# Optimization experiments

Measured on AMD Instinct MI355X. Metric: run time of the kernel, lower is better.

## Reference

```python
import jax, jax.numpy as jnp
import numpy as np

HID = 128      # hidden_dim
CDIM = 128     # c_dim
NBLK = 5       # n_blocks
RESO = 32      # grid_resolution
G = RESO ** 3  # number of voxels
B, T = 2, 100000


def setup_inputs() -> dict:
    key = jax.random.key(0)
    ks = jax.random.split(key, 8)
    return {
        "points": jax.random.normal(ks[0], (B, T, 3), jnp.float32),
        "index": jax.random.randint(ks[1], (B, 1, T), 0, G, dtype=jnp.int64),
        # fc_pos: Linear(3, 2*HID)
        "fc_pos_w": jax.random.normal(ks[2], (3, 2 * HID), jnp.float32) * 0.1,
        "fc_pos_b": jnp.zeros((2 * HID,), jnp.float32),
        # ResnetBlockFC(2*HID, HID) x NBLK: fc_0 (2H->H), fc_1 (H->H), shortcut (2H->H, no bias)
        "fc0_w": jax.random.normal(ks[3], (NBLK, 2 * HID, HID), jnp.float32) * 0.05,
        "fc0_b": jnp.zeros((NBLK, HID), jnp.float32),
        "fc1_w": jax.random.normal(ks[4], (NBLK, HID, HID), jnp.float32) * 0.05,
        "fc1_b": jnp.zeros((NBLK, HID), jnp.float32),
        "sc_w": jax.random.normal(ks[5], (NBLK, 2 * HID, HID), jnp.float32) * 0.05,
        # fc_c: Linear(HID, CDIM)
        "fc_c_w": jax.random.normal(ks[6], (HID, CDIM), jnp.float32) * 0.05,
        "fc_c_b": jnp.zeros((CDIM,), jnp.float32),
    }


def _resnet_block(x, w0, b0, w1, b1, ws):
    # ResnetBlockFC: net = fc_0(relu(x)); dx = fc_1(relu(net)); out = shortcut(x) + dx
    net = jnp.maximum(x, 0.0) @ w0 + b0
    dx = jnp.maximum(net, 0.0) @ w1 + b1
    return x @ ws + dx


def reference(points, index, fc_pos_w, fc_pos_b, fc0_w, fc0_b, fc1_w, fc1_b, sc_w, fc_c_w, fc_c_b):
    idx = index[:, 0, :]  # [B, T]

    def pool_local(net):
        # scatter_max over voxels, then gather back per point
        seg = jax.vmap(lambda c_b, i_b: jax.ops.segment_max(c_b, i_b, num_segments=G))(net, idx)  # [B,G,H]
        return jnp.take_along_axis(seg, idx[:, :, None], axis=1)  # [B,T,H]; every gathered voxel is non-empty

    net = points @ fc_pos_w + fc_pos_b          # [B,T,2H]
    net = _resnet_block(net, fc0_w[0], fc0_b[0], fc1_w[0], fc1_b[0], sc_w[0])  # [B,T,H]
    for i in range(1, NBLK):
        pooled = pool_local(net)
        net = jnp.concatenate([net, pooled], axis=2)  # [B,T,2H]
        net = _resnet_block(net, fc0_w[i], fc0_b[i], fc1_w[i], fc1_b[i], sc_w[i])

    c = net @ fc_c_w + fc_c_b  # [B,T,CDIM]

    # generate_grid_features: scatter_mean into the 32^3 grid (zeros for empty voxels)
    sums = jax.vmap(lambda c_b, i_b: jax.ops.segment_sum(c_b, i_b, num_segments=G))(c, idx)  # [B,G,CDIM]
    cnts = jax.vmap(lambda i_b: jax.ops.segment_sum(jnp.ones((T,), c.dtype), i_b, num_segments=G))(idx)  # [B,G]
    cnts = cnts[:, :, None]
    mean = jnp.where(cnts > 0, sums / jnp.maximum(cnts, 1.0), 0.0)
    fea_grid = jnp.transpose(mean, (0, 2, 1)).reshape(B, CDIM, RESO, RESO, RESO)
    return fea_grid
```

## Files before the change

### kernel.cpp

```cpp
#include <hip/hip_runtime.h>

#define T_PTS 100000
#define NB 2
#define NROWS (NB * T_PTS)
#define GCELLS 32768
#define NCELL (NB * GCELLS)
#define HID 128
#define MBLK 64
#define GRID_RB (NROWS / MBLK)

typedef __attribute__((ext_vector_type(8))) short bf16x8;
typedef __attribute__((ext_vector_type(4))) float f32x4;

#define MFMA16 __builtin_amdgcn_mfma_f32_16x16x32_bf16

__device__ __forceinline__ unsigned short bf16rne(float f) {
  unsigned u = __float_as_uint(f);
  return (unsigned short)((u + 0x7FFFu + ((u >> 16) & 1u)) >> 16);
}
__device__ __forceinline__ void bf16split(float f, unsigned short& h,
                                          unsigned short& l) {
  h = bf16rne(f);
  l = bf16rne(f - __uint_as_float(((unsigned)h) << 16));
}
__device__ __forceinline__ unsigned packhl(float f) {
  unsigned short h, l;
  bf16split(f, h, l);
  return (((unsigned)h) << 16) | (unsigned)l;
}

union U8 { bf16x8 v; unsigned u[4]; };

__device__ __forceinline__ void up2(unsigned w0, unsigned w1, unsigned& h,
                                    unsigned& l) {
  h = __builtin_amdgcn_perm(w1, w0, 0x07060302u);
  l = __builtin_amdgcn_perm(w1, w0, 0x05040100u);
}

__device__ __forceinline__ void relu2(unsigned qh, unsigned ql, unsigned& rh,
                                      unsigned& rl) {
  const unsigned keep = ((~qh >> 15) & 0x00010001u) * 0xFFFFu;
  rh = qh & keep;
  rl = ql & keep;
}

__device__ __forceinline__ void dma16(const unsigned* g, unsigned* l) {
  __builtin_amdgcn_global_load_lds(
      (const __attribute__((address_space(1))) unsigned*)g,
      (__attribute__((address_space(3))) unsigned*)l, 16, 0, 0);
}

template <int MODE>
__global__ __launch_bounds__(256, 4) void resblock_mfma(
    const void* __restrict__ srcv, const float* __restrict__ posw,
    const float* __restrict__ posb, const unsigned* __restrict__ cell,
    const int* __restrict__ perm, const int* __restrict__ vcell,
    const unsigned short* __restrict__ w0p, const float* __restrict__ b0,
    const unsigned short* __restrict__ w1p, const float* __restrict__ b1,
    const unsigned short* __restrict__ swp, unsigned* __restrict__ net_out) {
  __shared__ unsigned lds32[8192];
  const int tid = threadIdx.x;
  const int lane = tid & 63;
  const int wid = tid >> 6;
  const int wc = wid;
  const int t0 = blockIdx.x * MBLK;

  const int srow = wid * 16 + (lane & 15);
  const int skc4 = (lane >> 4) * 4;
  const long vrow = (long)t0 + srow;
  const unsigned* nrowL = nullptr;
  const unsigned* crowL = nullptr;
  float pp0 = 0.f, pp1 = 0.f, pp2 = 0.f;
  if (MODE == 1) {
    nrowL = (const unsigned*)srcv + vrow * HID;
    crowL = cell + (long)vcell[vrow] * HID;
  } else {
    const float* ppp = (const float*)srcv + (long)perm[vrow] * 3;
    pp0 = ppp[0]; pp1 = ppp[1]; pp2 = ppp[2];
  }

  auto stage_dma = [&](int ks) {
    unsigned* base = &lds32[((ks & 1) << 11) + wid * 256];
    const unsigned* rowp = (ks < 4) ? nrowL : crowL;
    const int ko = ((ks & 3) << 4) + skc4;
    dma16(rowp + ko, base);
    dma16(rowp + 64 + ko, base + 1024);
  };
  auto stage0 = [&](int ks) {
    const int kb = ks * 32 + (lane >> 4) * 8;
    float xv[8];
#pragma unroll
    for (int i = 0; i < 8; i += 4) {
      float4 wa = *(const float4*)(posw + kb + i);
      float4 wb = *(const float4*)(posw + 256 + kb + i);
      float4 wcc = *(const float4*)(posw + 512 + kb + i);
      float4 bb = *(const float4*)(posb + kb + i);
      xv[i + 0] = fmaf(pp0, wa.x, fmaf(pp1, wb.x, fmaf(pp2, wcc.x, bb.x)));
      xv[i + 1] = fmaf(pp0, wa.y, fmaf(pp1, wb.y, fmaf(pp2, wcc.y, bb.y)));
      xv[i + 2] = fmaf(pp0, wa.z, fmaf(pp1, wb.z, fmaf(pp2, wcc.z, bb.z)));
      xv[i + 3] = fmaf(pp0, wa.w, fmaf(pp1, wb.w, fmaf(pp2, wcc.w, bb.w)));
    }
    unsigned ph[8];
#pragma unroll
    for (int i = 0; i < 8; ++i) ph[i] = packhl(xv[i]);
    uint4 xh4, xl4;
    up2(ph[0], ph[1], xh4.x, xl4.x);
    up2(ph[2], ph[3], xh4.y, xl4.y);
    up2(ph[4], ph[5], xh4.z, xl4.z);
    up2(ph[6], ph[7], xh4.w, xl4.w);
    const int db = ((ks & 1) << 11) + wid * 256 + lane * 4;
    *(uint4*)&lds32[db] = xh4;
    *(uint4*)&lds32[db + 1024] = xl4;
  };
  auto load_B = [&](const unsigned short* base, int loOff, int ks, bf16x8* h,
                    bf16x8* l) {
#pragma unroll
    for (int nt = 0; nt < 2; ++nt) {
      const int fi = (ks * 8 + wc * 2 + nt) * 512 + lane * 8;
      h[nt] = *(const bf16x8*)(base + fi);
      l[nt] = *(const bf16x8*)(base + loOff + fi);
    }
  };

  f32x4 accy[4][2], acco[4][2];
#pragma unroll
  for (int i = 0; i < 4; ++i)
#pragma unroll
    for (int j = 0; j < 2; ++j) {
      f32x4 z = {0.f, 0.f, 0.f, 0.f};
      accy[i][j] = z;
      acco[i][j] = z;
    }

  if (MODE == 1) {
    stage_dma(0);
  } else {
    stage0(0);
  }
  __syncthreads();

#pragma unroll 1
  for (int ks = 0; ks < 8; ++ks) {
    const int sb = (ks & 1) << 11;
    bf16x8 b1h[2], b1l[2], b2h[2], b2l[2];
    load_B(w0p, 32768, ks, b1h, b1l);
    load_B(swp, 32768, ks, b2h, b2l);
    if (MODE == 1 && ks < 7) stage_dma(ks + 1);
    __builtin_amdgcn_s_setprio(1);
#pragma unroll
    for (int mt = 0; mt < 4; ++mt) {
      const unsigned* px = &lds32[sb + mt * 256 + lane * 4];
      U8 xh, xl, rh, rl;
      xh.v = *(const bf16x8*)px;
      xl.v = *(const bf16x8*)(px + 1024);
#pragma unroll
      for (int i = 0; i < 4; ++i) relu2(xh.u[i], xl.u[i], rh.u[i], rl.u[i]);
#pragma unroll
      for (int nt = 0; nt < 2; ++nt) {
        accy[mt][nt] = MFMA16(rh.v, b1h[nt], accy[mt][nt], 0, 0, 0);
        accy[mt][nt] = MFMA16(rh.v, b1l[nt], accy[mt][nt], 0, 0, 0);
        accy[mt][nt] = MFMA16(rl.v, b1h[nt], accy[mt][nt], 0, 0, 0);
      }
#pragma unroll
      for (int nt = 0; nt < 2; ++nt) {
        acco[mt][nt] = MFMA16(xh.v, b2h[nt], acco[mt][nt], 0, 0, 0);
        acco[mt][nt] = MFMA16(xh.v, b2l[nt], acco[mt][nt], 0, 0, 0);
        acco[mt][nt] = MFMA16(xl.v, b2h[nt], acco[mt][nt], 0, 0, 0);
      }
    }
    __builtin_amdgcn_s_setprio(0);
    if (MODE == 0 && ks < 7) stage0(ks + 1);
    __syncthreads();
  }

  {
    float b0v[2];
#pragma unroll
    for (int nt = 0; nt < 2; ++nt)
      b0v[nt] = b0[wc * 32 + nt * 16 + (lane & 15)];
#pragma unroll
    for (int mt = 0; mt < 4; ++mt) {
#pragma unroll
      for (int nt = 0; nt < 2; ++nt) {
        const int c = wc * 32 + nt * 16 + (lane & 15);
        const int k2 = c >> 5;
        const int j = c & 7;
        const int lahi = ((c & 31) >> 3) * 16;
#pragma unroll
        for (int r = 0; r < 4; ++r) {
          float h = fmaxf(accy[mt][nt][r] + b0v[nt], 0.f);
          int la = lahi + (lane >> 4) * 4 + r;
          la ^= (la >> 3) & 7;
          lds32[((k2 * 4 + mt) * 64 + la) * 8 + j] = packhl(h);
        }
      }
    }
  }
  __syncthreads();

  {
    const int lar2 = lane ^ ((lane >> 3) & 7);
#pragma unroll
    for (int k2 = 0; k2 < 4; ++k2) {
      bf16x8 ch[2], cl[2];
      load_B(w1p, 16384, k2, ch, cl);
      __builtin_amdgcn_s_setprio(1);
#pragma unroll
      for (int mt = 0; mt < 4; ++mt) {
        const unsigned* p = &lds32[((k2 * 4 + mt) * 64 + lar2) * 8];
        uint4 q1 = *(const uint4*)p;
        uint4 q2 = *(const uint4*)(p + 4);
        unsigned q[8] = {q1.x, q1.y, q1.z, q1.w, q2.x, q2.y, q2.z, q2.w};
        U8 ah, al;
#pragma unroll
        for (int p2 = 0; p2 < 4; ++p2)
          up2(q[2 * p2], q[2 * p2 + 1], ah.u[p2], al.u[p2]);
#pragma unroll
        for (int nt = 0; nt < 2; ++nt) {
          acco[mt][nt] = MFMA16(ah.v, ch[nt], acco[mt][nt], 0, 0, 0);
          acco[mt][nt] = MFMA16(ah.v, cl[nt], acco[mt][nt], 0, 0, 0);
          acco[mt][nt] = MFMA16(al.v, ch[nt], acco[mt][nt], 0, 0, 0);
        }
      }
      __builtin_amdgcn_s_setprio(0);
    }
  }

  {
    float b1v[2];
#pragma unroll
    for (int nt = 0; nt < 2; ++nt)
      b1v[nt] = b1[wc * 32 + nt * 16 + (lane & 15)];
#pragma unroll
    for (int mt = 0; mt < 4; ++mt) {
#pragma unroll
      for (int r = 0; r < 4; ++r) {
        const int row = mt * 16 + (lane >> 4) * 4 + r;
        unsigned short* op =
            (unsigned short*)(net_out + ((long)t0 + row) * HID);
        unsigned short h, l;
        bf16split(acco[mt][0][r] + b1v[0], h, l);
        op[wc * 32 + (lane & 15)] = h;
        op[128 + wc * 32 + (lane & 15)] = l;
        bf16split(acco[mt][1][r] + b1v[1], h, l);
        op[wc * 32 + 16 + (lane & 15)] = h;
        op[128 + wc * 32 + 16 + (lane & 15)] = l;
      }
    }
  }
}

__global__ __launch_bounds__(256, 4) void final_mfma(
    unsigned* __restrict__ net, const unsigned short* __restrict__ wcp,
    const float* __restrict__ bc) {
  __shared__ unsigned lds32[4096];
  const int tid = threadIdx.x;
  const int lane = tid & 63;
  const int wid = tid >> 6;
  const int wc = wid;
  const int t0 = blockIdx.x * MBLK;

  const int srow = wid * 16 + (lane & 15);
  const int skc4 = (lane >> 4) * 4;
  const unsigned* nrowL = net + ((long)t0 + srow) * HID;

  auto stage = [&](int ks) {
    unsigned* base = &lds32[((ks & 1) << 11) + wid * 256];
    const int ko = (ks << 4) + skc4;
    dma16(nrowL + ko, base);
    dma16(nrowL + 64 + ko, base + 1024);
  };
  auto load_B = [&](int ks, bf16x8* h, bf16x8* l) {
#pragma unroll
    for (int nt = 0; nt < 2; ++nt) {
      const int fi = (ks * 8 + wc * 2 + nt) * 512 + lane * 8;
      h[nt] = *(const bf16x8*)(wcp + fi);
      l[nt] = *(const bf16x8*)(wcp + 16384 + fi);
    }
  };

  f32x4 acc[4][2];
#pragma unroll
  for (int i = 0; i < 4; ++i)
#pragma unroll
    for (int j = 0; j < 2; ++j) {
      f32x4 z = {0.f, 0.f, 0.f, 0.f};
      acc[i][j] = z;
    }

  stage(0);
  __syncthreads();

#pragma unroll 1
  for (int ks = 0; ks < 4; ++ks) {
    const int sb = (ks & 1) << 11;
    bf16x8 ch[2], cl[2];
    load_B(ks, ch, cl);
    if (ks < 3) stage(ks + 1);
    __builtin_amdgcn_s_setprio(1);
#pragma unroll
    for (int mt = 0; mt < 4; ++mt) {
      const unsigned* px = &lds32[sb + mt * 256 + lane * 4];
      bf16x8 xh = *(const bf16x8*)px;
      bf16x8 xl = *(const bf16x8*)(px + 1024);
#pragma unroll
      for (int nt = 0; nt < 2; ++nt) {
        acc[mt][nt] = MFMA16(xh, ch[nt], acc[mt][nt], 0, 0, 0);
        acc[mt][nt] = MFMA16(xh, cl[nt], acc[mt][nt], 0, 0, 0);
        acc[mt][nt] = MFMA16(xl, ch[nt], acc[mt][nt], 0, 0, 0);
      }
    }
    __builtin_amdgcn_s_setprio(0);
    __syncthreads();
  }

  float* fout = (float*)net;
  float bcv[2];
#pragma unroll
  for (int nt = 0; nt < 2; ++nt)
    bcv[nt] = bc[wc * 32 + nt * 16 + (lane & 15)];
#pragma unroll
  for (int mt = 0; mt < 4; ++mt) {
#pragma unroll
    for (int r = 0; r < 4; ++r) {
      const int row = mt * 16 + (lane >> 4) * 4 + r;
      float* op = fout + ((long)t0 + row) * HID;
      op[wc * 32 + (lane & 15)] = acc[mt][0][r] + bcv[0];
      op[wc * 32 + 16 + (lane & 15)] = acc[mt][1][r] + bcv[1];
    }
  }
}

__global__ void pack_weights(const float* __restrict__ fc0,
                             const float* __restrict__ fc1,
                             const float* __restrict__ sc,
                             const float* __restrict__ fcc,
                             unsigned short* __restrict__ w0p,
                             unsigned short* __restrict__ w1p,
                             unsigned short* __restrict__ swp,
                             unsigned short* __restrict__ wcp) {
  int gid = blockIdx.x * 256 + threadIdx.x;
  const float* src;
  unsigned short* dst;
  int K, e;
  if (gid < 163840) { src = fc0; dst = w0p; K = 256; e = gid; }
  else if (gid < 327680) { src = sc; dst = swp; K = 256; e = gid - 163840; }
  else if (gid < 409600) { src = fc1; dst = w1p; K = 128; e = gid - 327680; }
  else if (gid < 425984) { src = fcc; dst = wcp; K = 128; e = gid - 409600; }
  else return;
  const int mat = e / (K * 128);
  const int r = e - mat * K * 128;
  const int k = r >> 7, n = r & 127;
  const float x = src[e];
  unsigned short hi, lo;
  bf16split(x, hi, lo);
  const int ks = k >> 5, lg = (k >> 3) & 3, j = k & 7;
  const int l = lg * 16 + (n & 15), nt = n >> 4;
  unsigned short* mb = dst + (long)mat * K * 256;
  const int off = ((ks * 8 + nt) * 64 + l) * 8 + j;
  mb[off] = hi;
  mb[off + K * 128] = lo;
}

__global__ void zero_i32(int* __restrict__ p, int n) {
  const int i = blockIdx.x * 256 + threadIdx.x;
  if (i < n) p[i] = 0;
}

__global__ void count_csr(const int* __restrict__ idx, int* __restrict__ curs) {
  const int gid = blockIdx.x * 256 + threadIdx.x;
  if (gid >= NROWS) return;
  const int b = gid / T_PTS;
  atomicAdd(&curs[b * GCELLS + idx[gid]], 1);
}

__global__ __launch_bounds__(1024) void scan_csr(const int* __restrict__ cnt,
                                                 int* __restrict__ offsets) {
  __shared__ int part[1024];
  const int t = threadIdx.x;
  const int base = t * (NCELL / 1024);
  int s = 0;
  for (int i = 0; i < NCELL / 1024; ++i) s += cnt[base + i];
  part[t] = s;
  __syncthreads();
  for (int d = 1; d < 1024; d <<= 1) {
    int v = (t >= d) ? part[t - d] : 0;
    __syncthreads();
    part[t] += v;
    __syncthreads();
  }
  int run = (t == 0) ? 0 : part[t - 1];
  for (int i = 0; i < NCELL / 1024; ++i) {
    offsets[base + i] = run;
    run += cnt[base + i];
  }
  if (t == 1023) offsets[NCELL] = run;
}

__global__ void scatter_csr(const int* __restrict__ idx,
                            const int* __restrict__ offsets,
                            int* __restrict__ curs, int* __restrict__ perm,
                            int* __restrict__ vcell) {
  const int gid = blockIdx.x * 256 + threadIdx.x;
  if (gid >= NROWS) return;
  const int b = gid / T_PTS;
  const int cellk = b * GCELLS + idx[gid];
  const int slot = offsets[cellk] + atomicAdd(&curs[cellk], 1);
  perm[slot] = gid;
  vcell[slot] = cellk;
}

__global__ __launch_bounds__(256) void pool_csr(const unsigned* __restrict__ net,
                                                const int* __restrict__ offsets,
                                                unsigned* __restrict__ cellf) {
  const int cellk = blockIdx.x * 4 + (threadIdx.x >> 6);
  const int lane = threadIdx.x & 63;
  const int s0 = offsets[cellk], s1 = offsets[cellk + 1];
  if (s0 >= s1) return;
  float m0 = -3.402823466e38f, m1 = -3.402823466e38f;
  unsigned h0 = 0u, l0 = 0u, h1 = 0u, l1 = 0u;
  for (int row = s0; row < s1; ++row) {
    const unsigned* rp = net + (long)row * HID;
    unsigned hi = rp[lane];
    unsigned lo = rp[64 + lane];
    float v0 = __uint_as_float(hi << 16) + __uint_as_float(lo << 16);
    float v1 = __uint_as_float(hi & 0xFFFF0000u) +
               __uint_as_float(lo & 0xFFFF0000u);
    if (v0 > m0) { m0 = v0; h0 = hi; l0 = lo; }
    if (v1 > m1) { m1 = v1; h1 = hi; l1 = lo; }
  }
  unsigned* cp = cellf + (long)cellk * HID;
  cp[lane] = (h0 & 0xFFFFu) | (h1 & 0xFFFF0000u);
  cp[64 + lane] = (l0 & 0xFFFFu) | (l1 & 0xFFFF0000u);
}

__global__ __launch_bounds__(256) void cellsum_csr(
    const float* __restrict__ c, const int* __restrict__ offsets,
    float* __restrict__ sums) {
  const int cellk = blockIdx.x * 4 + (threadIdx.x >> 6);
  const int lane = threadIdx.x & 63;
  const int s0 = offsets[cellk], s1 = offsets[cellk + 1];
  if (s0 >= s1) return;
  float2 m = {0.f, 0.f};
  for (int row = s0; row < s1; ++row) {
    float2 v = *(const float2*)(c + (long)row * HID + lane * 2);
    m.x += v.x;
    m.y += v.y;
  }
  *(float2*)(sums + (long)cellk * HID + lane * 2) = m;
}

__global__ void mean_kernel(const float* __restrict__ sums,
                            const int* __restrict__ offsets,
                            float* __restrict__ out) {
  const long gid = (long)blockIdx.x * 256 + threadIdx.x;
  if (gid >= (long)NB * HID * GCELLS) return;
  const int g = (int)(gid % GCELLS);
  const int c = (int)((gid / GCELLS) % HID);
  const int b = (int)(gid / ((long)HID * GCELLS));
  const int cellk = b * GCELLS + g;
  const int cnt = offsets[cellk + 1] - offsets[cellk];
  out[gid] = cnt > 0 ? sums[(long)cellk * HID + c] / (float)cnt : 0.f;
}

extern "C" void kernel_launch(void* const* d_in, const int* in_sizes, int n_in,
                              void* d_out, int out_size, void* d_ws,
                              size_t ws_size, hipStream_t stream) {
  const float* points = (const float*)d_in[0];
  const int* idx = (const int*)d_in[1];
  const float* fc_pos_w = (const float*)d_in[2];
  const float* fc_pos_b = (const float*)d_in[3];
  const float* fc0_w = (const float*)d_in[4];
  const float* fc0_b = (const float*)d_in[5];
  const float* fc1_w = (const float*)d_in[6];
  const float* fc1_b = (const float*)d_in[7];
  const float* sc_w = (const float*)d_in[8];
  const float* fc_c_w = (const float*)d_in[9];
  const float* fc_c_b = (const float*)d_in[10];
  float* out = (float*)d_out;

  const long NET_BYTES = (long)NROWS * HID * 4;
  const long CELL_BYTES = (long)NCELL * HID * 4;
  unsigned* net = (unsigned*)d_ws;
  unsigned* cellf = (unsigned*)((char*)d_ws + NET_BYTES);
  float* sums = (float*)cellf;
  int* offsets = (int*)((char*)d_ws + NET_BYTES + CELL_BYTES);

  unsigned short* packs = (unsigned short*)d_out;
  unsigned short* w0p = packs;
  unsigned short* swp = packs + 327680;
  unsigned short* w1p = packs + 655360;
  unsigned short* wcp = packs + 819200;
  int* curs = (int*)((char*)d_out + (2l << 20));
  int* perm = (int*)((char*)d_out + (3l << 20));
  int* vcell = (int*)((char*)d_out + (4l << 20));

  const int GRID_PTS = (NROWS + 255) / 256;
  const int GRID_ZERO = (NCELL + 255) / 256;
  const int GRID_CELL = NCELL / 4;
  const int GRID_MEAN = NB * HID * GCELLS / 256;

  pack_weights<<<1664, 256, 0, stream>>>(fc0_w, fc1_w, sc_w, fc_c_w, w0p, w1p,
                                         swp, wcp);

  zero_i32<<<GRID_ZERO, 256, 0, stream>>>(curs, NCELL);
  count_csr<<<GRID_PTS, 256, 0, stream>>>(idx, curs);
  scan_csr<<<1, 1024, 0, stream>>>(curs, offsets);
  zero_i32<<<GRID_ZERO, 256, 0, stream>>>(curs, NCELL);
  scatter_csr<<<GRID_PTS, 256, 0, stream>>>(idx, offsets, curs, perm, vcell);

  resblock_mfma<0><<<GRID_RB, 256, 0, stream>>>(
      points, fc_pos_w, fc_pos_b, nullptr, perm, vcell, w0p, fc0_b, w1p,
      fc1_b, swp, net);

  for (int i = 1; i < 5; ++i) {
    pool_csr<<<GRID_CELL, 256, 0, stream>>>(net, offsets, cellf);
    resblock_mfma<1><<<GRID_RB, 256, 0, stream>>>(
        net, nullptr, nullptr, cellf, perm, vcell, w0p + (long)i * 65536,
        fc0_b + i * HID, w1p + (long)i * 32768, fc1_b + i * HID,
        swp + (long)i * 65536, net);
  }

  final_mfma<<<GRID_RB, 256, 0, stream>>>(net, wcp, fc_c_b);
  cellsum_csr<<<GRID_CELL, 256, 0, stream>>>((const float*)net, offsets, sums);
  mean_kernel<<<GRID_MEAN, 256, 0, stream>>>(sums, offsets, out);
}
```

Baseline: 755.3 us.

## Use 8-wave blocks with full-tile LDS staging in resblock and final GEMMs

The resblock and final MFMA kernels now launch 512 threads (8 waves), and each wave owns 16 output columns instead of 32. The per-k-step double-buffered staging loop is replaced by a single up-front load of the whole 64-row input tile into a larger LDS buffer, which removes the per-step barriers. The aim is more waves per block to hide latency and fewer synchronisations. In exchange the kernels use twice the LDS, get lower occupancy per CU, no longer overlap loads with MFMA work, and each wave loads its B fragments with less reuse.

```diff
diff --git a/kernel.cpp b/kernel.cpp
--- a/kernel.cpp
+++ b/kernel.cpp
@@ -51,13 +51,185 @@
 }
 
 template <int MODE>
-__global__ __launch_bounds__(256, 4) void resblock_mfma(
+__global__ __launch_bounds__(512, 2) void resblock_mfma(
     const void* __restrict__ srcv, const float* __restrict__ posw,
     const float* __restrict__ posb, const unsigned* __restrict__ cell,
     const int* __restrict__ perm, const int* __restrict__ vcell,
     const unsigned short* __restrict__ w0p, const float* __restrict__ b0,
     const unsigned short* __restrict__ w1p, const float* __restrict__ b1,
     const unsigned short* __restrict__ swp, unsigned* __restrict__ net_out) {
+  __shared__ unsigned lds32[16384];
+  const int tid = threadIdx.x;
+  const int lane = tid & 63;
+  const int wid = tid >> 6;
+  const int wc = wid;
+  const int t0 = blockIdx.x * MBLK;
+
+  if (MODE == 1) {
+    const int plane = wid >> 2;
+    const int mtreg = wid & 3;
+    const long vrow = (long)t0 + mtreg * 16 + (lane & 15);
+    const unsigned* nrowL =
+        (const unsigned*)srcv + vrow * HID + plane * 64;
+    const unsigned* crowL = cell + (long)vcell[vrow] * HID + plane * 64;
+    const int lo4 = (lane >> 4) * 4;
+#pragma unroll
+    for (int ks = 0; ks < 8; ++ks) {
+      const unsigned* src =
+          ((ks < 4) ? nrowL + ks * 16 : crowL + (ks - 4) * 16) + lo4;
+      dma16(src, &lds32[ks * 2048 + plane * 1024 + mtreg * 256]);
+    }
+  } else {
+    const int row = tid >> 3;
+    const int ks = tid & 7;
+    const float* ppp = (const float*)srcv + (long)perm[(long)t0 + row] * 3;
+    const float p0 = ppp[0], p1 = ppp[1], p2 = ppp[2];
+    const int kb = ks * 32;
+    float xv[32];
+#pragma unroll
+    for (int i = 0; i < 32; i += 4) {
+      float4 wa = *(const float4*)(posw + kb + i);
+      float4 wb = *(const float4*)(posw + 256 + kb + i);
+      float4 wcc = *(const float4*)(posw + 512 + kb + i);
+      float4 bb = *(const float4*)(posb + kb + i);
+      xv[i + 0] = fmaf(p0, wa.x, fmaf(p1, wb.x, fmaf(p2, wcc.x, bb.x)));
+      xv[i + 1] = fmaf(p0, wa.y, fmaf(p1, wb.y, fmaf(p2, wcc.y, bb.y)));
+      xv[i + 2] = fmaf(p0, wa.z, fmaf(p1, wb.z, fmaf(p2, wcc.z, bb.z)));
+      xv[i + 3] = fmaf(p0, wa.w, fmaf(p1, wb.w, fmaf(p2, wcc.w, bb.w)));
+    }
+    unsigned hu[16], lu[16];
+#pragma unroll
+    for (int c = 0; c < 16; ++c) {
+      unsigned short h0, l0, h1, l1;
+      bf16split(xv[2 * c], h0, l0);
+      bf16split(xv[2 * c + 1], h1, l1);
+      hu[c] = (unsigned)h0 | ((unsigned)h1 << 16);
+      lu[c] = (unsigned)l0 | ((unsigned)l1 << 16);
+    }
+    const int rb = ks * 2048 + (row >> 4) * 256;
+#pragma unroll
+    for (int kq = 0; kq < 4; ++kq) {
+      const int o = rb + (kq * 16 + (row & 15)) * 4;
+      uint4 q;
+      q.x = hu[kq * 4]; q.y = hu[kq * 4 + 1];
+      q.z = hu[kq * 4 + 2]; q.w = hu[kq * 4 + 3];
+      *(uint4*)&lds32[o] = q;
+      q.x = lu[kq * 4]; q.y = lu[kq * 4 + 1];
+      q.z = lu[kq * 4 + 2]; q.w = lu[kq * 4 + 3];
+      *(uint4*)&lds32[o + 1024] = q;
+    }
+  }
+
+  f32x4 accy[4], acco[4];
+#pragma unroll
+  for (int i = 0; i < 4; ++i) {
+    f32x4 z = {0.f, 0.f, 0.f, 0.f};
+    accy[i] = z;
+    acco[i] = z;
+  }
+
+  __syncthreads();
+
+#pragma unroll 1
+  for (int ks = 0; ks < 8; ++ks) {
+    bf16x8 b1h, b1l, b2h, b2l;
+    {
+      const int fi = (ks * 8 + wc) * 512 + lane * 8;
+      b1h = *(const bf16x8*)(w0p + fi);
+      b1l = *(const bf16x8*)(w0p + 32768 + fi);
+      b2h = *(const bf16x8*)(swp + fi);
+      b2l = *(const bf16x8*)(swp + 32768 + fi);
+    }
+    __builtin_amdgcn_s_setprio(1);
+#pragma unroll
+    for (int mt = 0; mt < 4; ++mt) {
+      const unsigned* px = &lds32[ks * 2048 + mt * 256 + lane * 4];
+      U8 xh, xl, rh, rl;
+      xh.v = *(const bf16x8*)px;
+      xl.v = *(const bf16x8*)(px + 1024);
+#pragma unroll
+      for (int i = 0; i < 4; ++i) relu2(xh.u[i], xl.u[i], rh.u[i], rl.u[i]);
+      accy[mt] = MFMA16(rh.v, b1h, accy[mt], 0, 0, 0);
+      accy[mt] = MFMA16(rh.v, b1l, accy[mt], 0, 0, 0);
+      accy[mt] = MFMA16(rl.v, b1h, accy[mt], 0, 0, 0);
+      acco[mt] = MFMA16(xh.v, b2h, acco[mt], 0, 0, 0);
+      acco[mt] = MFMA16(xh.v, b2l, acco[mt], 0, 0, 0);
+      acco[mt] = MFMA16(xl.v, b2h, acco[mt], 0, 0, 0);
+    }
+    __builtin_amdgcn_s_setprio(0);
+  }
+  __syncthreads();
+
+  {
+    const int c = wc * 16 + (lane & 15);
+    const float b0v = b0[c];
+    const int k2 = c >> 5;
+    const int j = c & 7;
+    const int lahi = ((c & 31) >> 3) * 16;
+#pragma unroll
+    for (int mt = 0; mt < 4; ++mt) {
+#pragma unroll
+      for (int r = 0; r < 4; ++r) {
+        float h = fmaxf(accy[mt][r] + b0v, 0.f);
+        int la = lahi + (lane >> 4) * 4 + r;
+        la ^= (la >> 3) & 7;
+        lds32[((k2 * 4 + mt) * 64 + la) * 8 + j] = packhl(h);
+      }
+    }
+  }
+  __syncthreads();
+
+  {
+    const int lar2 = lane ^ ((lane >> 3) & 7);
+#pragma unroll
+    for (int k2 = 0; k2 < 4; ++k2) {
+      bf16x8 ch, cl;
+      {
+        const int fi = (k2 * 8 + wc) * 512 + lane * 8;
+        ch = *(const bf16x8*)(w1p + fi);
+        cl = *(const bf16x8*)(w1p + 16384 + fi);
+      }
+      __builtin_amdgcn_s_setprio(1);
+#pragma unroll
+      for (int mt = 0; mt < 4; ++mt) {
+        const unsigned* p = &lds32[((k2 * 4 + mt) * 64 + lar2) * 8];
+        uint4 q1 = *(const uint4*)p;
+        uint4 q2 = *(const uint4*)(p + 4);
+        unsigned q[8] = {q1.x, q1.y, q1.z, q1.w, q2.x, q2.y, q2.z, q2.w};
+        U8 ah, al;
+#pragma unroll
+        for (int p2 = 0; p2 < 4; ++p2)
+          up2(q[2 * p2], q[2 * p2 + 1], ah.u[p2], al.u[p2]);
+        acco[mt] = MFMA16(ah.v, ch, acco[mt], 0, 0, 0);
+        acco[mt] = MFMA16(ah.v, cl, acco[mt], 0, 0, 0);
+        acco[mt] = MFMA16(al.v, ch, acco[mt], 0, 0, 0);
+      }
+      __builtin_amdgcn_s_setprio(0);
+    }
+  }
+
+  {
+    const int c = wc * 16 + (lane & 15);
+    const float b1v = b1[c];
+#pragma unroll
+    for (int mt = 0; mt < 4; ++mt) {
+#pragma unroll
+      for (int r = 0; r < 4; ++r) {
+        const int row = mt * 16 + (lane >> 4) * 4 + r;
+        unsigned short* op =
+            (unsigned short*)(net_out + ((long)t0 + row) * HID);
+        unsigned short h, l;
+        bf16split(acco[mt][r] + b1v, h, l);
+        op[c] = h;
+        op[128 + c] = l;
+      }
+    }
+  }
+}
+
+__global__ __launch_bounds__(512, 2) void final_mfma(
+    unsigned* __restrict__ net, const unsigned short* __restrict__ wcp,
+    const float* __restrict__ bc) {
   __shared__ unsigned lds32[8192];
   const int tid = threadIdx.x;
   const int lane = tid & 63;
@@ -65,268 +237,57 @@
   const int wc = wid;
   const int t0 = blockIdx.x * MBLK;
 
-  const int srow = wid * 16 + (lane & 15);
-  const int skc4 = (lane >> 4) * 4;
-  const long vrow = (long)t0 + srow;
-  const unsigned* nrowL = nullptr;
-  const unsigned* crowL = nullptr;
-  float pp0 = 0.f, pp1 = 0.f, pp2 = 0.f;
-  if (MODE == 1) {
-    nrowL = (const unsigned*)srcv + vrow * HID;
-    crowL = cell + (long)vcell[vrow] * HID;
-  } else {
-    const float* ppp = (const float*)srcv + (long)perm[vrow] * 3;
-    pp0 = ppp[0]; pp1 = ppp[1]; pp2 = ppp[2];
-  }
-
-  auto stage_dma = [&](int ks) {
-    unsigned* base = &lds32[((ks & 1) << 11) + wid * 256];
-    const unsigned* rowp = (ks < 4) ? nrowL : crowL;
-    const int ko = ((ks & 3) << 4) + skc4;
-    dma16(rowp + ko, base);
-    dma16(rowp + 64 + ko, base + 1024);
-  };
-  auto stage0 = [&](int ks) {
-    const int kb = ks * 32 + (lane >> 4) * 8;
-    float xv[8];
-#pragma unroll
-    for (int i = 0; i < 8; i += 4) {
-      float4 wa = *(const float4*)(posw + kb + i);
-      float4 wb = *(const float4*)(posw + 256 + kb + i);
-      float4 wcc = *(const float4*)(posw + 512 + kb + i);
-      float4 bb = *(const float4*)(posb + kb + i);
-      xv[i + 0] = fmaf(pp0, wa.x, fmaf(pp1, wb.x, fmaf(pp2, wcc.x, bb.x)));
-      xv[i + 1] = fmaf(pp0, wa.y, fmaf(pp1, wb.y, fmaf(pp2, wcc.y, bb.y)));
-      xv[i + 2] = fmaf(pp0, wa.z, fmaf(pp1, wb.z, fmaf(pp2, wcc.z, bb.z)));
-      xv[i + 3] = fmaf(pp0, wa.w, fmaf(pp1, wb.w, fmaf(pp2, wcc.w, bb.w)));
-    }
-    unsigned ph[8];
-#pragma unroll
-    for (int i = 0; i < 8; ++i) ph[i] = packhl(xv[i]);
-    uint4 xh4, xl4;
-    up2(ph[0], ph[1], xh4.x, xl4.x);
-    up2(ph[2], ph[3], xh4.y, xl4.y);
-    up2(ph[4], ph[5], xh4.z, xl4.z);
-    up2(ph[6], ph[7], xh4.w, xl4.w);
-    const int db = ((ks & 1) << 11) + wid * 256 + lane * 4;
-    *(uint4*)&lds32[db] = xh4;
-    *(uint4*)&lds32[db + 1024] = xl4;
-  };
-  auto load_B = [&](const unsigned short* base, int loOff, int ks, bf16x8* h,
-                    bf16x8* l) {
-#pragma unroll
-    for (int nt = 0; nt < 2; ++nt) {
-      const int fi = (ks * 8 + wc * 2 + nt) * 512 + lane * 8;
-      h[nt] = *(const bf16x8*)(base + fi);
-      l[nt] = *(const bf16x8*)(base + loOff + fi);
-    }
-  };
-
-  f32x4 accy[4][2], acco[4][2];
-#pragma unroll
-  for (int i = 0; i < 4; ++i)
-#pragma unroll
-    for (int j = 0; j < 2; ++j) {
-      f32x4 z = {0.f, 0.f, 0.f, 0.f};
-      accy[i][j] = z;
-      acco[i][j] = z;
-    }
-
-  if (MODE == 1) {
-    stage_dma(0);
-  } else {
-    stage0(0);
-  }
-  __syncthreads();
-
-#pragma unroll 1
-  for (int ks = 0; ks < 8; ++ks) {
-    const int sb = (ks & 1) << 11;
-    bf16x8 b1h[2], b1l[2], b2h[2], b2l[2];
-    load_B(w0p, 32768, ks, b1h, b1l);
-    load_B(swp, 32768, ks, b2h, b2l);
-    if (MODE == 1 && ks < 7) stage_dma(ks + 1);
-    __builtin_amdgcn_s_setprio(1);
-#pragma unroll
-    for (int mt = 0; mt < 4; ++mt) {
-      const unsigned* px = &lds32[sb + mt * 256 + lane * 4];
-      U8 xh, xl, rh, rl;
-      xh.v = *(const bf16x8*)px;
-      xl.v = *(const bf16x8*)(px + 1024);
-#pragma unroll
-      for (int i = 0; i < 4; ++i) relu2(xh.u[i], xl.u[i], rh.u[i], rl.u[i]);
-#pragma unroll
-      for (int nt = 0; nt < 2; ++nt) {
-        accy[mt][nt] = MFMA16(rh.v, b1h[nt], accy[mt][nt], 0, 0, 0);
-        accy[mt][nt] = MFMA16(rh.v, b1l[nt], accy[mt][nt], 0, 0, 0);
-        accy[mt][nt] = MFMA16(rl.v, b1h[nt], accy[mt][nt], 0, 0, 0);
-      }
-#pragma unroll
-      for (int nt = 0; nt < 2; ++nt) {
-        acco[mt][nt] = MFMA16(xh.v, b2h[nt], acco[mt][nt], 0, 0, 0);
-        acco[mt][nt] = MFMA16(xh.v, b2l[nt], acco[mt][nt], 0, 0, 0);
-        acco[mt][nt] = MFMA16(xl.v, b2h[nt], acco[mt][nt], 0, 0, 0);
-      }
-    }
-    __builtin_amdgcn_s_setprio(0);
-    if (MODE == 0 && ks < 7) stage0(ks + 1);
-    __syncthreads();
-  }
-
   {
-    float b0v[2];
-#pragma unroll
-    for (int nt = 0; nt < 2; ++nt)
-      b0v[nt] = b0[wc * 32 + nt * 16 + (lane & 15)];
-#pragma unroll
-    for (int mt = 0; mt < 4; ++mt) {
-#pragma unroll
-      for (int nt = 0; nt < 2; ++nt) {
-        const int c = wc * 32 + nt * 16 + (lane & 15);
-        const int k2 = c >> 5;
-        const int j = c & 7;
-        const int lahi = ((c & 31) >> 3) * 16;
-#pragma unroll
-        for (int r = 0; r < 4; ++r) {
-          float h = fmaxf(accy[mt][nt][r] + b0v[nt], 0.f);
-          int la = lahi + (lane >> 4) * 4 + r;
-          la ^= (la >> 3) & 7;
-          lds32[((k2 * 4 + mt) * 64 + la) * 8 + j] = packhl(h);
-        }
-      }
-    }
-  }
-  __syncthreads();
-
-  {
-    const int lar2 = lane ^ ((lane >> 3) & 7);
-#pragma unroll
-    for (int k2 = 0; k2 < 4; ++k2) {
-      bf16x8 ch[2], cl[2];
-      load_B(w1p, 16384, k2, ch, cl);
-      __builtin_amdgcn_s_setprio(1);
-#pragma unroll
-      for (int mt = 0; mt < 4; ++mt) {
-        const unsigned* p = &lds32[((k2 * 4 + mt) * 64 + lar2) * 8];
-        uint4 q1 = *(const uint4*)p;
-        uint4 q2 = *(const uint4*)(p + 4);
-        unsigned q[8] = {q1.x, q1.y, q1.z, q1.w, q2.x, q2.y, q2.z, q2.w};
-        U8 ah, al;
-#pragma unroll
-        for (int p2 = 0; p2 < 4; ++p2)
-          up2(q[2 * p2], q[2 * p2 + 1], ah.u[p2], al.u[p2]);
-#pragma unroll
-        for (int nt = 0; nt < 2; ++nt) {
-          acco[mt][nt] = MFMA16(ah.v, ch[nt], acco[mt][nt], 0, 0, 0);
-          acco[mt][nt] = MFMA16(ah.v, cl[nt], acco[mt][nt], 0, 0, 0);
-          acco[mt][nt] = MFMA16(al.v, ch[nt], acco[mt][nt], 0, 0, 0);
-        }
-      }
-      __builtin_amdgcn_s_setprio(0);
-    }
-  }
-
-  {
-    float b1v[2];
-#pragma unroll
-    for (int nt = 0; nt < 2; ++nt)
-      b1v[nt] = b1[wc * 32 + nt * 16 + (lane & 15)];
-#pragma unroll
-    for (int mt = 0; mt < 4; ++mt) {
-#pragma unroll
-      for (int r = 0; r < 4; ++r) {
-        const int row = mt * 16 + (lane >> 4) * 4 + r;
-        unsigned short* op =
-            (unsigned short*)(net_out + ((long)t0 + row) * HID);
-        unsigned short h, l;
-        bf16split(acco[mt][0][r] + b1v[0], h, l);
-        op[wc * 32 + (lane & 15)] = h;
-        op[128 + wc * 32 + (lane & 15)] = l;
-        bf16split(acco[mt][1][r] + b1v[1], h, l);
-        op[wc * 32 + 16 + (lane & 15)] = h;
-        op[128 + wc * 32 + 16 + (lane & 15)] = l;
-      }
-    }
-  }
-}
-
-__global__ __launch_bounds__(256, 4) void final_mfma(
-    unsigned* __restrict__ net, const unsigned short* __restrict__ wcp,
-    const float* __restrict__ bc) {
-  __shared__ unsigned lds32[4096];
-  const int tid = threadIdx.x;
-  const int lane = tid & 63;
-  const int wid = tid >> 6;
-  const int wc = wid;
-  const int t0 = blockIdx.x * MBLK;
-
-  const int srow = wid * 16 + (lane & 15);
-  const int skc4 = (lane >> 4) * 4;
-  const unsigned* nrowL = net + ((long)t0 + srow) * HID;
-
-  auto stage = [&](int ks) {
-    unsigned* base = &lds32[((ks & 1) << 11) + wid * 256];
-    const int ko = (ks << 4) + skc4;
-    dma16(nrowL + ko, base);
-    dma16(nrowL + 64 + ko, base + 1024);
-  };
-  auto load_B = [&](int ks, bf16x8* h, bf16x8* l) {
-#pragma unroll
-    for (int nt = 0; nt < 2; ++nt) {
-      const int fi = (ks * 8 + wc * 2 + nt) * 512 + lane * 8;
-      h[nt] = *(const bf16x8*)(wcp + fi);
-      l[nt] = *(const bf16x8*)(wcp + 16384 + fi);
-    }
-  };
-
-  f32x4 acc[4][2];
-#pragma unroll
-  for (int i = 0; i < 4; ++i)
-#pragma unroll
-    for (int j = 0; j < 2; ++j) {
-      f32x4 z = {0.f, 0.f, 0.f, 0.f};
-      acc[i][j] = z;
-    }
-
-  stage(0);
+    const int plane = wid >> 2;
+    const int mtreg = wid & 3;
+    const long vrow = (long)t0 + mtreg * 16 + (lane & 15);
+    const unsigned* nrowL = net + vrow * HID + plane * 64;
+    const int lo4 = (lane >> 4) * 4;
+#pragma unroll
+    for (int ks = 0; ks < 4; ++ks)
+      dma16(nrowL + ks * 16 + lo4,
+            &lds32[ks * 2048 + plane * 1024 + mtreg * 256]);
+  }
+
+  f32x4 acc[4];
+#pragma unroll
+  for (int i = 0; i < 4; ++i) {
+    f32x4 z = {0.f, 0.f, 0.f, 0.f};
+    acc[i] = z;
+  }
+
   __syncthreads();
 
 #pragma unroll 1
   for (int ks = 0; ks < 4; ++ks) {
-    const int sb = (ks & 1) << 11;
-    bf16x8 ch[2], cl[2];
-    load_B(ks, ch, cl);
-    if (ks < 3) stage(ks + 1);
+    bf16x8 ch, cl;
+    {
+      const int fi = (ks * 8 + wc) * 512 + lane * 8;
+      ch = *(const bf16x8*)(wcp + fi);
+      cl = *(const bf16x8*)(wcp + 16384 + fi);
+    }
     __builtin_amdgcn_s_setprio(1);
 #pragma unroll
     for (int mt = 0; mt < 4; ++mt) {
-      const unsigned* px = &lds32[sb + mt * 256 + lane * 4];
+      const unsigned* px = &lds32[ks * 2048 + mt * 256 + lane * 4];
       bf16x8 xh = *(const bf16x8*)px;
       bf16x8 xl = *(const bf16x8*)(px + 1024);
-#pragma unroll
-      for (int nt = 0; nt < 2; ++nt) {
-        acc[mt][nt] = MFMA16(xh, ch[nt], acc[mt][nt], 0, 0, 0);
-        acc[mt][nt] = MFMA16(xh, cl[nt], acc[mt][nt], 0, 0, 0);
-        acc[mt][nt] = MFMA16(xl, ch[nt], acc[mt][nt], 0, 0, 0);
-      }
+      acc[mt] = MFMA16(xh, ch, acc[mt], 0, 0, 0);
+      acc[mt] = MFMA16(xh, cl, acc[mt], 0, 0, 0);
+      acc[mt] = MFMA16(xl, ch, acc[mt], 0, 0, 0);
     }
     __builtin_amdgcn_s_setprio(0);
-    __syncthreads();
   }
 
   float* fout = (float*)net;
-  float bcv[2];
-#pragma unroll
-  for (int nt = 0; nt < 2; ++nt)
-    bcv[nt] = bc[wc * 32 + nt * 16 + (lane & 15)];
+  const int c = wc * 16 + (lane & 15);
+  const float bcv = bc[c];
 #pragma unroll
   for (int mt = 0; mt < 4; ++mt) {
 #pragma unroll
     for (int r = 0; r < 4; ++r) {
       const int row = mt * 16 + (lane >> 4) * 4 + r;
-      float* op = fout + ((long)t0 + row) * HID;
-      op[wc * 32 + (lane & 15)] = acc[mt][0][r] + bcv[0];
-      op[wc * 32 + 16 + (lane & 15)] = acc[mt][1][r] + bcv[1];
+      fout[((long)t0 + row) * HID + c] = acc[mt][r] + bcv;
     }
   }
 }
@@ -509,19 +470,19 @@
   zero_i32<<<GRID_ZERO, 256, 0, stream>>>(curs, NCELL);
   scatter_csr<<<GRID_PTS, 256, 0, stream>>>(idx, offsets, curs, perm, vcell);
 
-  resblock_mfma<0><<<GRID_RB, 256, 0, stream>>>(
+  resblock_mfma<0><<<GRID_RB, 512, 0, stream>>>(
       points, fc_pos_w, fc_pos_b, nullptr, perm, vcell, w0p, fc0_b, w1p,
       fc1_b, swp, net);
 
   for (int i = 1; i < 5; ++i) {
     pool_csr<<<GRID_CELL, 256, 0, stream>>>(net, offsets, cellf);
-    resblock_mfma<1><<<GRID_RB, 256, 0, stream>>>(
+    resblock_mfma<1><<<GRID_RB, 512, 0, stream>>>(
         net, nullptr, nullptr, cellf, perm, vcell, w0p + (long)i * 65536,
         fc0_b + i * HID, w1p + (long)i * 32768, fc1_b + i * HID,
         swp + (long)i * 65536, net);
   }
 
-  final_mfma<<<GRID_RB, 256, 0, stream>>>(net, wcp, fc_c_b);
+  final_mfma<<<GRID_RB, 512, 0, stream>>>(net, wcp, fc_c_b);
   cellsum_csr<<<GRID_CELL, 256, 0, stream>>>((const float*)net, offsets, sums);
   mean_kernel<<<GRID_MEAN, 256, 0, stream>>>(sums, offsets, out);
 }
```

Measured after the change: 875.9 us. 16.0% more time.
